# Optimization experiments

Hardware: AMD Instinct MI355X
Metric: run time of the kernel (lower is better)

## Reference

```python
import jax, jax.numpy as jnp
import numpy as np

B, T, D, H, O = 64, 2048, 64, 512, 128


def setup_inputs() -> dict:
    key = jax.random.key(0)
    ks = jax.random.split(key, 7)
    s = 1.0 / np.sqrt(H).astype(np.float32)  # PyTorch default uniform(-1/sqrt(H), 1/sqrt(H))
    u = lambda k, shp: jax.random.uniform(k, shp, jnp.float32, -s, s)
    return {
        "x": jax.random.normal(ks[0], (B, T, D), jnp.float32),
        "W_ih": u(ks[1], (4 * H, D)),
        "W_hh": u(ks[2], (4 * H, H)),
        "b_ih": u(ks[3], (4 * H,)),
        "b_hh": u(ks[4], (4 * H,)),
        "W_out": u(ks[5], (O, H)),
        "b_out": u(ks[6], (O,)),
        "batch_size": B,
    }


def reference(x, W_ih, W_hh, b_ih, b_hh, W_out, b_out, batch_size):
    Bv, Tv, Dv = x.shape
    Hv = W_hh.shape[1]
    # Precompute input-to-gate projections for all timesteps: [T, B, 4H]
    xg = (jnp.einsum("btd,gd->btg", x, W_ih) + b_ih + b_hh).transpose(1, 0, 2)
    h0 = jnp.zeros((Bv, Hv), x.dtype)
    c0 = jnp.zeros((Bv, Hv), x.dtype)

    def step(carry, g_t):
        h, c = carry
        g = g_t + h @ W_hh.T  # [B, 4H]
        i, f, gc, o = jnp.split(g, 4, axis=-1)  # PyTorch gate order i,f,g,o
        i = jax.nn.sigmoid(i)
        f = jax.nn.sigmoid(f)
        gc = jnp.tanh(gc)
        o = jax.nn.sigmoid(o)
        c = f * c + i * gc
        h = o * jnp.tanh(c)
        return (h, c), None

    (hT, cT), _ = jax.lax.scan(step, (h0, c0), xg)
    # Linear applied at last timestep only (module returns predictions[:, -1, :])
    pred = hT @ W_out.T + b_out  # [B, O]
    return pred, hT[None], cT[None]  # (pred, h_n[1,B,H], c_n[1,B,H])
```

## Files before the change

### kernel.cpp

```cpp
#include <hip/hip_runtime.h>
#include <hip/hip_bf16.h>


typedef short short8 __attribute__((ext_vector_type(8)));
typedef float floatx4 __attribute__((ext_vector_type(4)));

#define T_STEPS 2048
#define NBG 4
#define NGI 32
#define SB() __builtin_amdgcn_sched_barrier(0)

__device__ __forceinline__ unsigned short f2bf(float f){
    unsigned u = __builtin_bit_cast(unsigned, f);
    u += 0x7FFFu + ((u >> 16) & 1u);
    return (unsigned short)(u >> 16);
}

__device__ __forceinline__ short8 pack8(float4 a, float4 b){
    short8 s;
    s[0]=(short)f2bf(a.x); s[1]=(short)f2bf(a.y); s[2]=(short)f2bf(a.z); s[3]=(short)f2bf(a.w);
    s[4]=(short)f2bf(b.x); s[5]=(short)f2bf(b.y); s[6]=(short)f2bf(b.z); s[7]=(short)f2bf(b.w);
    return s;
}

__device__ __forceinline__ float fsigmoid(float x){ return 1.0f/(1.0f+__expf(-x)); }
__device__ __forceinline__ float ftanh(float x){ return 2.0f*fsigmoid(2.0f*x)-1.0f; }

__device__ __forceinline__ void hload16_dev(short8* A, const unsigned short* base){
    asm volatile(
    "global_load_dwordx4 %0, %16, off sc1\n\t"
    "global_load_dwordx4 %1, %16, off offset:64 sc1\n\t"
    "global_load_dwordx4 %2, %16, off offset:128 sc1\n\t"
    "global_load_dwordx4 %3, %16, off offset:192 sc1\n\t"
    "global_load_dwordx4 %4, %16, off offset:256 sc1\n\t"
    "global_load_dwordx4 %5, %16, off offset:320 sc1\n\t"
    "global_load_dwordx4 %6, %16, off offset:384 sc1\n\t"
    "global_load_dwordx4 %7, %16, off offset:448 sc1\n\t"
    "global_load_dwordx4 %8, %16, off offset:512 sc1\n\t"
    "global_load_dwordx4 %9, %16, off offset:576 sc1\n\t"
    "global_load_dwordx4 %10, %16, off offset:640 sc1\n\t"
    "global_load_dwordx4 %11, %16, off offset:704 sc1\n\t"
    "global_load_dwordx4 %12, %16, off offset:768 sc1\n\t"
    "global_load_dwordx4 %13, %16, off offset:832 sc1\n\t"
    "global_load_dwordx4 %14, %16, off offset:896 sc1\n\t"
    "global_load_dwordx4 %15, %16, off offset:960 sc1"
    : "=&v"(A[0]), "=&v"(A[1]), "=&v"(A[2]), "=&v"(A[3]),
      "=&v"(A[4]), "=&v"(A[5]), "=&v"(A[6]), "=&v"(A[7]),
      "=&v"(A[8]), "=&v"(A[9]), "=&v"(A[10]), "=&v"(A[11]),
      "=&v"(A[12]), "=&v"(A[13]), "=&v"(A[14]), "=&v"(A[15])
    : "v"(base) : "memory");
}

__global__ __launch_bounds__(64, 1)
void lstm_persist(const float* __restrict__ x,
                  const float* __restrict__ W_ih,
                  const float* __restrict__ W_hh,
                  const float* __restrict__ b_ih,
                  const float* __restrict__ b_hh,
                  const float* __restrict__ W_out,
                  const float* __restrict__ b_out,
                  float* __restrict__ out,
                  unsigned short* __restrict__ hbuf)
{
    const int wg   = blockIdx.x;
    const int bg   = wg & 3;
    const int gi   = wg >> 2;
    const int lane = threadIdx.x;
    const int ln   = lane & 15;
    const int lk   = lane >> 4;
    const int hd0  = gi << 4;

    __shared__ __align__(16) unsigned short hl[256];

    short8 bw[4][18];
#pragma unroll
    for (int g = 0; g < 4; ++g){
        const int row = g * 512 + hd0 + ln;
        const float* pih = W_ih + row * 64 + lk * 8;
#pragma unroll
        for (int kk = 0; kk < 2; ++kk){
            float4 u0 = *reinterpret_cast<const float4*>(pih + kk * 32);
            float4 u1 = *reinterpret_cast<const float4*>(pih + kk * 32 + 4);
            bw[g][kk] = pack8(u0, u1);
        }
        const float* phh = W_hh + row * 512 + lk * 8;
#pragma unroll
        for (int kk = 2; kk < 18; ++kk){
            float4 u0 = *reinterpret_cast<const float4*>(phh + (kk - 2) * 32);
            float4 u1 = *reinterpret_cast<const float4*>(phh + (kk - 2) * 32 + 4);
            bw[g][kk] = pack8(u0, u1);
        }
    }

    float bias[4];
#pragma unroll
    for (int g = 0; g < 4; ++g){
        const int col = g * 512 + hd0 + ln;
        bias[g] = b_ih[col] + b_hh[col];
    }

    float c0 = 0.f, c1 = 0.f, c2 = 0.f, c3 = 0.f;
    const int xrow = bg * 16 + ln;

    for (int t = 0; t < T_STEPS; ++t){
        const float* xp = x + ((size_t)xrow * T_STEPS + (size_t)t) * 64 + lk * 8;
        float4 x0a = *reinterpret_cast<const float4*>(xp);
        float4 x0b = *reinterpret_cast<const float4*>(xp + 4);
        float4 x1a = *reinterpret_cast<const float4*>(xp + 32);
        float4 x1b = *reinterpret_cast<const float4*>(xp + 36);

        short8 a[18];
        a[0] = pack8(x0a, x0b);
        a[1] = pack8(x1a, x1b);

        floatx4 acc0 = {bias[0], bias[0], bias[0], bias[0]};
        floatx4 acc1 = {bias[1], bias[1], bias[1], bias[1]};
        floatx4 acc2 = {bias[2], bias[2], bias[2], bias[2]};
        floatx4 acc3 = {bias[3], bias[3], bias[3], bias[3]};

#pragma unroll
        for (int kk = 0; kk < 2; ++kk){
            acc0 = __builtin_amdgcn_mfma_f32_16x16x32_bf16(a[kk], bw[0][kk], acc0, 0, 0, 0);
            acc1 = __builtin_amdgcn_mfma_f32_16x16x32_bf16(a[kk], bw[1][kk], acc1, 0, 0, 0);
            acc2 = __builtin_amdgcn_mfma_f32_16x16x32_bf16(a[kk], bw[2][kk], acc2, 0, 0, 0);
            acc3 = __builtin_amdgcn_mfma_f32_16x16x32_bf16(a[kk], bw[3][kk], acc3, 0, 0, 0);
        }

        if (t > 0){
            const unsigned expst = (((unsigned)(t - 1) >> 1) & 1u) + 1u;
            const unsigned short* hp =
                hbuf + (size_t)((((t & 1) ^ 1) * NBG + bg) * 16 + ln) * 512 + lk * 8;
            int ok;
            do {
                hload16_dev(&a[2], hp);
                asm volatile("s_waitcnt vmcnt(0)" ::: "memory");
                SB();
                ok = 1;
#pragma unroll
                for (int kk = 2; kk < 18; ++kk){
                    unsigned s = ((unsigned)(unsigned short)a[kk][6] & 1u)
                               | (((unsigned)(unsigned short)a[kk][7] & 1u) << 1);
                    ok &= (s == expst) ? 1 : 0;
                }
            } while (!__all(ok));
            SB();
        } else {
#pragma unroll
            for (int kk = 2; kk < 18; ++kk){
                short8 z = {0,0,0,0,0,0,0,0};
                a[kk] = z;
            }
        }

#pragma unroll
        for (int kk = 2; kk < 18; ++kk){
            acc0 = __builtin_amdgcn_mfma_f32_16x16x32_bf16(a[kk], bw[0][kk], acc0, 0, 0, 0);
            acc1 = __builtin_amdgcn_mfma_f32_16x16x32_bf16(a[kk], bw[1][kk], acc1, 0, 0, 0);
            acc2 = __builtin_amdgcn_mfma_f32_16x16x32_bf16(a[kk], bw[2][kk], acc2, 0, 0, 0);
            acc3 = __builtin_amdgcn_mfma_f32_16x16x32_bf16(a[kk], bw[3][kk], acc3, 0, 0, 0);
        }

#define EPI(R, CREG)                                                         \
        {   float iv = fsigmoid(acc0[R]);                                    \
            float fv_ = fsigmoid(acc1[R]);                                   \
            float gv = ftanh(acc2[R]);                                       \
            float ov = fsigmoid(acc3[R]);                                    \
            CREG = fv_ * CREG + iv * gv;                                     \
            float hv = ov * ftanh(CREG);                                     \
            hl[(lk * 4 + R) * 16 + ln] = f2bf(hv);                           \
            if (t == T_STEPS - 1){                                           \
                int rr = bg * 16 + lk * 4 + R;                               \
                out[8192  + rr * 512 + hd0 + ln] = hv;                       \
                out[40960 + rr * 512 + hd0 + ln] = CREG;                     \
            }                                                                \
        }
        EPI(0, c0) EPI(1, c1) EPI(2, c2) EPI(3, c3)
#undef EPI

        asm volatile("s_waitcnt lgkmcnt(0)" ::: "memory");

        {
            const unsigned stamp = (((unsigned)t >> 1) & 1u) + 1u;
            if (lane < 32){
                const int row = lane >> 1, half = lane & 1;
                short8 v = *reinterpret_cast<const short8*>(&hl[row * 16 + half * 8]);
                v[6] = (short)((v[6] & ~(short)1) | (short)(stamp & 1u));
                v[7] = (short)((v[7] & ~(short)1) | (short)((stamp >> 1) & 1u));
                unsigned short* dst =
                    hbuf + (size_t)(((t & 1) * NBG + bg) * 16 + row) * 512 + hd0 + half * 8;
                asm volatile("global_store_dwordx4 %0, %1, off sc1"
                             :: "v"(dst), "v"(v) : "memory");
            }
            asm volatile("s_waitcnt vmcnt(0)" ::: "memory");
        }
    }

    if (gi == 0){
        const unsigned expst = (((unsigned)(T_STEPS - 1) >> 1) & 1u) + 1u;
        const unsigned short* hp =
            hbuf + (size_t)((((T_STEPS - 1) & 1) * NBG + bg) * 16 + ln) * 512 + lk * 8;
        short8 ha[16];
        int ok;
        do {
            hload16_dev(ha, hp);
            asm volatile("s_waitcnt vmcnt(0)" ::: "memory");
            SB();
            ok = 1;
#pragma unroll
            for (int kk = 0; kk < 16; ++kk){
                unsigned s = ((unsigned)(unsigned short)ha[kk][6] & 1u)
                           | (((unsigned)(unsigned short)ha[kk][7] & 1u) << 1);
                ok &= (s == expst) ? 1 : 0;
            }
        } while (!__all(ok));
        SB();
#pragma unroll
        for (int o0 = 0; o0 < 8; ++o0){
            const int col = o0 * 16 + ln;
            const float* wp = W_out + col * 512 + lk * 8;
            floatx4 pa = {0.f, 0.f, 0.f, 0.f};
#pragma unroll
            for (int kk = 0; kk < 16; ++kk){
                float4 w0 = *reinterpret_cast<const float4*>(wp + kk * 32);
                float4 w1 = *reinterpret_cast<const float4*>(wp + kk * 32 + 4);
                pa = __builtin_amdgcn_mfma_f32_16x16x32_bf16(ha[kk], pack8(w0, w1), pa, 0, 0, 0);
            }
            const float bo = b_out[col];
#pragma unroll
            for (int r = 0; r < 4; ++r){
                const int rr = bg * 16 + lk * 4 + r;
                out[rr * 128 + col] = pa[r] + bo;
            }
        }
    }
}

extern "C" void kernel_launch(void* const* d_in, const int* in_sizes, int n_in,
                              void* d_out, int out_size, void* d_ws, size_t ws_size,
                              hipStream_t stream) {
    const float* x     = (const float*)d_in[0];
    const float* W_ih  = (const float*)d_in[1];
    const float* W_hh  = (const float*)d_in[2];
    const float* b_ih  = (const float*)d_in[3];
    const float* b_hh  = (const float*)d_in[4];
    const float* W_out = (const float*)d_in[5];
    const float* b_out = (const float*)d_in[6];

    const size_t HBUF_BYTES = (size_t)2 * NBG * 16 * 512 * 2;
    unsigned short* hbuf = (unsigned short*)d_ws;

    hipMemsetAsync(hbuf, 0, HBUF_BYTES, stream);
    lstm_persist<<<dim3(NBG * NGI), dim3(64), 0, stream>>>(
        x, W_ih, W_hh, b_ih, b_hh, W_out, b_out,
        (float*)d_out, hbuf);
}
```

Baseline: 7.694 ms.

## Prefetch next-step inputs and consume hidden-state chunks as they arrive

Each step now issues the next step's hidden-state load and input-row load right after the epilogue, instead of at the top of the next step. The polling loop checks each of the 16 hidden-state chunks separately and runs the MFMAs for every chunk whose stamp already matches, then reloads only while some chunks are still pending. The aim is to hide global-memory latency and cross-block synchronisation wait on the serial recurrence. The cost is a more complex, divergent polling loop, and the speculative first load may often read stale data and have to be repeated.

```diff
diff --git a/kernel.cpp b/kernel.cpp
--- a/kernel.cpp
+++ b/kernel.cpp
@@ -7,7 +7,6 @@
 
 #define T_STEPS 2048
 #define NBG 4
-#define NGI 32
 #define SB() __builtin_amdgcn_sched_barrier(0)
 
 __device__ __forceinline__ unsigned short f2bf(float f){
@@ -102,16 +101,16 @@
     float c0 = 0.f, c1 = 0.f, c2 = 0.f, c3 = 0.f;
     const int xrow = bg * 16 + ln;
 
+    short8 a[18];
+    const float* xp0 = x + ((size_t)xrow * T_STEPS) * 64 + lk * 8;
+    float4 xr0a = *reinterpret_cast<const float4*>(xp0);
+    float4 xr0b = *reinterpret_cast<const float4*>(xp0 + 4);
+    float4 xr1a = *reinterpret_cast<const float4*>(xp0 + 32);
+    float4 xr1b = *reinterpret_cast<const float4*>(xp0 + 36);
+
     for (int t = 0; t < T_STEPS; ++t){
-        const float* xp = x + ((size_t)xrow * T_STEPS + (size_t)t) * 64 + lk * 8;
-        float4 x0a = *reinterpret_cast<const float4*>(xp);
-        float4 x0b = *reinterpret_cast<const float4*>(xp + 4);
-        float4 x1a = *reinterpret_cast<const float4*>(xp + 32);
-        float4 x1b = *reinterpret_cast<const float4*>(xp + 36);
-
-        short8 a[18];
-        a[0] = pack8(x0a, x0b);
-        a[1] = pack8(x1a, x1b);
+        a[0] = pack8(xr0a, xr0b);
+        a[1] = pack8(xr1a, xr1b);
 
         floatx4 acc0 = {bias[0], bias[0], bias[0], bias[0]};
         floatx4 acc1 = {bias[1], bias[1], bias[1], bias[1]};
@@ -130,34 +129,30 @@
             const unsigned expst = (((unsigned)(t - 1) >> 1) & 1u) + 1u;
             const unsigned short* hp =
                 hbuf + (size_t)((((t & 1) ^ 1) * NBG + bg) * 16 + ln) * 512 + lk * 8;
-            int ok;
-            do {
-                hload16_dev(&a[2], hp);
+            unsigned pend = 0xFFFFu;
+            for (;;){
                 asm volatile("s_waitcnt vmcnt(0)" ::: "memory");
                 SB();
-                ok = 1;
-#pragma unroll
-                for (int kk = 2; kk < 18; ++kk){
-                    unsigned s = ((unsigned)(unsigned short)a[kk][6] & 1u)
-                               | (((unsigned)(unsigned short)a[kk][7] & 1u) << 1);
-                    ok &= (s == expst) ? 1 : 0;
+                unsigned ready = 0;
+#pragma unroll
+                for (int c = 0; c < 16; ++c){
+                    if (pend & (1u << c)){
+                        unsigned s = ((unsigned)(unsigned short)a[c + 2][6] & 1u)
+                                   | (((unsigned)(unsigned short)a[c + 2][7] & 1u) << 1);
+                        if (__all((int)(s == expst))){
+                            ready |= 1u << c;
+                            acc0 = __builtin_amdgcn_mfma_f32_16x16x32_bf16(a[c+2], bw[0][c+2], acc0, 0, 0, 0);
+                            acc1 = __builtin_amdgcn_mfma_f32_16x16x32_bf16(a[c+2], bw[1][c+2], acc1, 0, 0, 0);
+                            acc2 = __builtin_amdgcn_mfma_f32_16x16x32_bf16(a[c+2], bw[2][c+2], acc2, 0, 0, 0);
+                            acc3 = __builtin_amdgcn_mfma_f32_16x16x32_bf16(a[c+2], bw[3][c+2], acc3, 0, 0, 0);
+                        }
+                    }
                 }
-            } while (!__all(ok));
+                pend &= ~ready;
+                if (!pend) break;
+                hload16_dev(&a[2], hp);
+            }
             SB();
-        } else {
-#pragma unroll
-            for (int kk = 2; kk < 18; ++kk){
-                short8 z = {0,0,0,0,0,0,0,0};
-                a[kk] = z;
-            }
-        }
-
-#pragma unroll
-        for (int kk = 2; kk < 18; ++kk){
-            acc0 = __builtin_amdgcn_mfma_f32_16x16x32_bf16(a[kk], bw[0][kk], acc0, 0, 0, 0);
-            acc1 = __builtin_amdgcn_mfma_f32_16x16x32_bf16(a[kk], bw[1][kk], acc1, 0, 0, 0);
-            acc2 = __builtin_amdgcn_mfma_f32_16x16x32_bf16(a[kk], bw[2][kk], acc2, 0, 0, 0);
-            acc3 = __builtin_amdgcn_mfma_f32_16x16x32_bf16(a[kk], bw[3][kk], acc3, 0, 0, 0);
         }
 
 #define EPI(R, CREG)                                                         \
@@ -177,6 +172,20 @@
         EPI(0, c0) EPI(1, c1) EPI(2, c2) EPI(3, c3)
 #undef EPI
 
+        {
+            const unsigned short* hpn =
+                hbuf + (size_t)(((t & 1) * NBG + bg) * 16 + ln) * 512 + lk * 8;
+            hload16_dev(&a[2], hpn);
+        }
+        {
+            const int tn = (t + 1 < T_STEPS) ? (t + 1) : t;
+            const float* xp = x + ((size_t)xrow * T_STEPS + (size_t)tn) * 64 + lk * 8;
+            xr0a = *reinterpret_cast<const float4*>(xp);
+            xr0b = *reinterpret_cast<const float4*>(xp + 4);
+            xr1a = *reinterpret_cast<const float4*>(xp + 32);
+            xr1b = *reinterpret_cast<const float4*>(xp + 36);
+        }
+
         asm volatile("s_waitcnt lgkmcnt(0)" ::: "memory");
 
         {
@@ -192,6 +201,7 @@
                              :: "v"(dst), "v"(v) : "memory");
             }
             asm volatile("s_waitcnt vmcnt(0)" ::: "memory");
+            SB();
         }
     }
 
@@ -250,7 +260,7 @@
     unsigned short* hbuf = (unsigned short*)d_ws;
 
     hipMemsetAsync(hbuf, 0, HBUF_BYTES, stream);
-    lstm_persist<<<dim3(NBG * NGI), dim3(64), 0, stream>>>(
+    lstm_persist<<<dim3(NBG * 32), dim3(64), 0, stream>>>(
         x, W_ih, W_hh, b_ih, b_hh, W_out, b_out,
         (float*)d_out, hbuf);
 }
```

New measurement: 8.391 ms. +9.1%, slower.
